# Performance work log

Hardware: AMD Instinct MI355X
Metric: run time of the kernel (lower is better)

## Reference

```python
import jax, jax.numpy as jnp
import numpy as np

N = 50000      # nodes
E = 800000     # edges
MUL = 32       # multiplicity of each irrep (32x0e + 32x1o)
SQRT3 = 3.0 ** 0.5


def setup_inputs() -> dict:
    key = jax.random.key(0)
    k = jax.random.split(key, 7)
    node_features = jax.random.normal(k[0], (N, 4 * MUL), dtype=jnp.float32)  # [N, 32 + 32*3]
    positions = jax.random.normal(k[1], (N, 3), dtype=jnp.float32)
    edge_src = jax.random.randint(k[2], (E,), 0, N, dtype=jnp.int32)
    edge_dst = jax.random.randint(k[3], (E,), 0, N, dtype=jnp.int32)
    tp_weight = jax.random.normal(k[4], (4 * MUL,), dtype=jnp.float32)  # tp.weight_numel = 128
    W_s = jax.random.normal(k[5], (2 * MUL, MUL), dtype=jnp.float32)    # linear: mid 0e (2 blocks) -> out 0e
    W_v = jax.random.normal(k[6], (2 * MUL, MUL), dtype=jnp.float32)    # linear: mid 1o (2 blocks) -> out 1o
    return dict(node_features=node_features, positions=positions,
                edge_src=edge_src, edge_dst=edge_dst,
                tp_weight=tp_weight, W_s=W_s, W_v=W_v)


def reference(node_features, positions, edge_src, edge_dst, tp_weight, W_s, W_v):
    # --- edge vectors and spherical harmonics (normalize=True, 'component') ---
    edge_vec = positions[edge_dst] - positions[edge_src]                       # [E,3]
    unit = edge_vec * jax.lax.rsqrt(jnp.sum(edge_vec * edge_vec, -1, keepdims=True) + 1e-12)
    sh1 = SQRT3 * unit                                                         # l=1 SH, component norm; sh0 == 1
    # --- gather source node features, split irreps ---
    src = node_features[edge_src]                                              # [E,128]
    s = src[:, :MUL]                                                           # [E,32]  scalars 32x0e
    v = src[:, MUL:].reshape(-1, MUL, 3)                                       # [E,32,3] vectors 32x1o
    w0, w1, w2, w3 = jnp.split(tp_weight, 4)                                   # per-path 'uvu' weights (u=32, v=1)
    # --- CG tensor product paths ---
    mid0 = w0 * s                                                              # 0e x 0e -> 0e
    mid1 = (w1 * s)[:, :, None] * sh1[:, None, :]                              # 0e x 1o -> 1o
    mid2 = w2[None, :, None] * v                                               # 1o x 0e -> 1o
    mid3 = w3 * (jnp.einsum('eum,em->eu', v, sh1) / SQRT3)                     # 1o x 1o -> 0e (w3j = delta/sqrt(3))
    messages = jnp.concatenate(
        [mid0, mid1.reshape(-1, 3 * MUL), mid2.reshape(-1, 3 * MUL), mid3], axis=-1)  # [E,256]
    # --- scatter-add messages to destination nodes ---
    agg = jax.ops.segment_sum(messages, edge_dst, num_segments=N)              # [N,256]
    a0 = agg[:, :MUL]
    a1 = agg[:, MUL:4 * MUL].reshape(N, MUL, 3)
    a2 = agg[:, 4 * MUL:7 * MUL].reshape(N, MUL, 3)
    a3 = agg[:, 7 * MUL:]
    # --- equivariant linear mix mid -> out (fan-in normalized per irrep) ---
    inv = np.float32(1.0 / np.sqrt(2 * MUL))
    out_s = (jnp.concatenate([a0, a3], axis=-1) @ W_s) * inv                   # [N,32]
    out_v = jnp.einsum('num,uo->nom', jnp.concatenate([a1, a2], axis=1), W_v) * inv  # [N,32,3]
    return jnp.concatenate([out_s, out_v.reshape(N, 3 * MUL)], axis=-1)        # [N,128]
```

## Files before the change

### kernel.cpp

```cpp
#include <hip/hip_runtime.h>
#include <hip/hip_fp16.h>

#define SQRT3 1.7320508075688772f
#define INV_SQRT3 0.5773502691896258f
#define CAP 64

#define WAVE_SYNC() do { asm volatile("s_waitcnt lgkmcnt(0)" ::: "memory"); \
                         __builtin_amdgcn_wave_barrier(); } while (0)

__global__ void prep_kernel(const float* __restrict__ feat, const float* __restrict__ pos,
                            const float* __restrict__ Ws, const float* __restrict__ Wv,
                            const float* __restrict__ tpw,
                            uint2* __restrict__ featH, float4* __restrict__ pos4,
                            int* __restrict__ cnt,
                            __half2* __restrict__ WS2, __half2* __restrict__ WV2, int N) {
    int i = blockIdx.x * blockDim.x + threadIdx.x;
    int totalF = N * 32;
    if (i < totalF) {
        int node = i >> 5, cl = i & 31;
        const float* fb = feat + (size_t)node * 128;
        float s  = fb[cl];
        float v0 = fb[32 + 3 * cl], v1 = fb[33 + 3 * cl], v2 = fb[34 + 3 * cl];
        __half2 h0 = __floats2half2_rn(s, v0);
        __half2 h1 = __floats2half2_rn(v1, v2);
        uint2 r;
        r.x = *(const unsigned int*)&h0;
        r.y = *(const unsigned int*)&h1;
        featH[i] = r;
        return;
    }
    int j = i - totalF;
    if (j < N) {
        pos4[j] = make_float4(pos[3 * j], pos[3 * j + 1], pos[3 * j + 2], 0.f);
        cnt[j] = 0;
        return;
    }
    int k = j - N;
    if (k < 1024) {
        int u2 = k >> 5, c = k & 31;
        int ua = 2 * u2, ub = 2 * u2 + 1;
        auto fs = [&](int u) {
            float w = Ws[u * 32 + c];
            return (u < 32) ? 0.125f * tpw[u] * w
                            : 0.125f * tpw[96 + (u - 32)] * INV_SQRT3 * w;
        };
        auto fv = [&](int u) {
            float w = Wv[u * 32 + c];
            return (u < 32) ? 0.125f * tpw[32 + u] * w
                            : 0.125f * tpw[64 + (u - 32)] * w;
        };
        WS2[k] = __floats2half2_rn(fs(ua), fs(ub));
        WV2[k] = __floats2half2_rn(fv(ua), fv(ub));
    }
}

__global__ void scatter_kernel(const int* __restrict__ esrc, const int* __restrict__ edst,
                               int* __restrict__ cnt, int* __restrict__ csrP, int E) {
    int t = blockIdx.x * blockDim.x + threadIdx.x;
    int e0 = t * 4;
    if (e0 + 4 <= E) {
        int4 s4 = *(const int4*)(esrc + e0);
        int4 d4 = *(const int4*)(edst + e0);
        int p;
        p = atomicAdd(&cnt[d4.x], 1); if (p < CAP) csrP[(size_t)d4.x * CAP + p] = s4.x;
        p = atomicAdd(&cnt[d4.y], 1); if (p < CAP) csrP[(size_t)d4.y * CAP + p] = s4.y;
        p = atomicAdd(&cnt[d4.z], 1); if (p < CAP) csrP[(size_t)d4.z * CAP + p] = s4.z;
        p = atomicAdd(&cnt[d4.w], 1); if (p < CAP) csrP[(size_t)d4.w * CAP + p] = s4.w;
    } else {
        for (int e = e0; e < E; ++e) {
            int d = edst[e];
            int p = atomicAdd(&cnt[d], 1);
            if (p < CAP) csrP[(size_t)d * CAP + p] = esrc[e];
        }
    }
}


__global__ __launch_bounds__(256) void node_kernel(
    const uint2* __restrict__ featH, const float4* __restrict__ pos4,
    const int* __restrict__ csrP, const int* __restrict__ cnt,
    const __half2* __restrict__ WS2, const __half2* __restrict__ WV2,
    float* __restrict__ out, int N)
{
    __shared__ float4 geom[4][64];
    __shared__ float  sS[4][68], sX[4][68], sY[4][68], sZ[4][68];
    int lane = threadIdx.x & 63;
    int w    = threadIdx.x >> 6;
    int node = blockIdx.x * 4 + w;
    if (node >= N) return;

    int deg = cnt[node];
    int len = deg < CAP ? deg : CAP;
    int half = lane >> 5;
    int cl   = lane & 31;

    float4 pd = pos4[node];

    if (lane < len) {
        int s = csrP[(size_t)node * CAP + lane];
        float4 ps = pos4[s];
        float ex = pd.x - ps.x, ey = pd.y - ps.y, ez = pd.z - ps.z;
        float rr = SQRT3 * rsqrtf(ex * ex + ey * ey + ez * ez + 1e-12f);
        geom[w][lane] = make_float4(rr * ex, rr * ey, rr * ez, __int_as_float(s));
    }
    WAVE_SYNC();

    float A0 = 0.f, A1x = 0.f, A1y = 0.f, A1z = 0.f;
    float V0 = 0.f, V1 = 0.f, V2 = 0.f, T3 = 0.f;

    int even = len & ~1;
    #pragma unroll 4
    for (int m = 0; m < even; m += 2) {
        float4 g = geom[w][m + half];
        int si = __float_as_int(g.w);
        uint2 fr = featH[(size_t)si * 32 + cl];
        float2 lo = __half22float2(*(const __half2*)&fr.x);
        float2 hi = __half22float2(*(const __half2*)&fr.y);
        A0 += lo.x;
        A1x = fmaf(lo.x, g.x, A1x); A1y = fmaf(lo.x, g.y, A1y); A1z = fmaf(lo.x, g.z, A1z);
        V0 += lo.y; V1 += hi.x; V2 += hi.y;
        T3 = fmaf(lo.y, g.x, fmaf(hi.x, g.y, fmaf(hi.y, g.z, T3)));
    }
    if (len & 1) {
        if (half == 0) {
            float4 g = geom[w][len - 1];
            int si = __float_as_int(g.w);
            uint2 fr = featH[(size_t)si * 32 + cl];
            float2 lo = __half22float2(*(const __half2*)&fr.x);
            float2 hi = __half22float2(*(const __half2*)&fr.y);
            A0 += lo.x;
            A1x = fmaf(lo.x, g.x, A1x); A1y = fmaf(lo.x, g.y, A1y); A1z = fmaf(lo.x, g.z, A1z);
            V0 += lo.y; V1 += hi.x; V2 += hi.y;
            T3 = fmaf(lo.y, g.x, fmaf(hi.x, g.y, fmaf(hi.y, g.z, T3)));
        }
    }

    A0 += __shfl_xor(A0, 32);  A1x += __shfl_xor(A1x, 32);
    A1y += __shfl_xor(A1y, 32); A1z += __shfl_xor(A1z, 32);
    V0 += __shfl_xor(V0, 32);  V1 += __shfl_xor(V1, 32);
    V2 += __shfl_xor(V2, 32);  T3 += __shfl_xor(T3, 32);

    int k = half ? (32 + cl) : cl;
    sS[w][k] = half ? T3 : A0;
    sX[w][k] = half ? V0 : A1x;
    sY[w][k] = half ? V1 : A1y;
    sZ[w][k] = half ? V2 : A1z;
    WAVE_SYNC();

    size_t ob = (size_t)node * 128;
    #pragma unroll
    for (int t = 0; t < 2; ++t) {
        int j = lane + 64 * t;
        const float *ap;
        const __half2 *wp2;
        if (j < 32) {
            ap = sS[w]; wp2 = WS2 + j;
        } else {
            int v = j - 32;
            int o = v / 3, mm = v - 3 * o;
            ap = (mm == 0) ? sX[w] : (mm == 1) ? sY[w] : sZ[w];
            wp2 = WV2 + o;
        }
        float r = 0.f;
        #pragma unroll
        for (int q = 0; q < 16; ++q) {
            float4 a = *(const float4*)(ap + 4 * q);
            float2 w0 = __half22float2(wp2[(2 * q)     * 32]);
            float2 w1 = __half22float2(wp2[(2 * q + 1) * 32]);
            r = fmaf(a.x, w0.x, r); r = fmaf(a.y, w0.y, r);
            r = fmaf(a.z, w1.x, r); r = fmaf(a.w, w1.y, r);
        }
        out[ob + j] = r;
    }
}

extern "C" void kernel_launch(void* const* d_in, const int* in_sizes, int n_in,
                              void* d_out, int out_size, void* d_ws, size_t ws_size,
                              hipStream_t stream) {
    const float* feat = (const float*)d_in[0];
    const float* pos  = (const float*)d_in[1];
    const int*   esrc = (const int*)d_in[2];
    const int*   edst = (const int*)d_in[3];
    const float* tpw  = (const float*)d_in[4];
    const float* Ws   = (const float*)d_in[5];
    const float* Wv   = (const float*)d_in[6];
    float* out = (float*)d_out;

    int N = in_sizes[0] / 128;
    int E = in_sizes[2];

    uint2*   featH = (uint2*)d_ws;
    float4*  pos4  = (float4*)(featH + (size_t)N * 32);
    int*     csrP  = (int*)(pos4 + N);
    int*     cnt   = csrP + (size_t)N * CAP;
    __half2* WS2   = (__half2*)(cnt + N);
    __half2* WV2   = WS2 + 1024;

    const int tb = 256;
    int prepTot = N * 32 + N + 1024;
    int ebk = (E / 4 + tb) / tb;
    prep_kernel<<<(prepTot + tb - 1) / tb, tb, 0, stream>>>(feat, pos, Ws, Wv, tpw,
                                                            featH, pos4, cnt, WS2, WV2, N);
    scatter_kernel<<<ebk, tb, 0, stream>>>(esrc, edst, cnt, csrP, E);
    node_kernel<<<(N + 3) / 4, 256, 0, stream>>>(featH, pos4, csrP, cnt, WS2, WV2, out, N);
}
```

Baseline: 107.5 us.

## Process two destination nodes per wave with zero-padded gather loop

Each wave now handles two destination nodes at once. Edge lists are padded to a multiple of 8 using a dummy zero feature row at index N, so the inner loop runs without odd-length tails and issues two independent feature gathers per iteration. This raises memory-level parallelism and removes divergent tail handling. In exchange it does wasted work when the two nodes have unequal degrees, uses more registers and shared memory, and halves the number of blocks.

```diff
diff --git a/kernel.cpp b/kernel.cpp
--- a/kernel.cpp
+++ b/kernel.cpp
@@ -30,6 +30,8 @@
         return;
     }
     int j = i - totalF;
+    if (j < 32) { featH[totalF + j] = make_uint2(0u, 0u); return; }
+    j -= 32;
     if (j < N) {
         pos4[j] = make_float4(pos[3 * j], pos[3 * j + 1], pos[3 * j + 2], 0.f);
         cnt[j] = 0;
@@ -82,95 +84,127 @@
     const __half2* __restrict__ WS2, const __half2* __restrict__ WV2,
     float* __restrict__ out, int N)
 {
-    __shared__ float4 geom[4][64];
-    __shared__ float  sS[4][68], sX[4][68], sY[4][68], sZ[4][68];
+    __shared__ float4 geom[4][2][64];
+    __shared__ float  sS[4][2][68], sX[4][2][68], sY[4][2][68], sZ[4][2][68];
     int lane = threadIdx.x & 63;
     int w    = threadIdx.x >> 6;
-    int node = blockIdx.x * 4 + w;
-    if (node >= N) return;
-
-    int deg = cnt[node];
-    int len = deg < CAP ? deg : CAP;
+    int n0   = blockIdx.x * 8 + 2 * w;
+    if (n0 >= N) return;
+    int n1   = n0 + 1;
+    bool has1 = n1 < N;
+
+    int len0 = cnt[n0]; len0 = len0 < CAP ? len0 : CAP;
+    int len1 = 0;
+    if (has1) { len1 = cnt[n1]; len1 = len1 < CAP ? len1 : CAP; }
+    int lmax = len0 > len1 ? len0 : len1;
+    int lenP = (lmax + 7) & ~7;
     int half = lane >> 5;
     int cl   = lane & 31;
 
-    float4 pd = pos4[node];
-
-    if (lane < len) {
-        int s = csrP[(size_t)node * CAP + lane];
-        float4 ps = pos4[s];
-        float ex = pd.x - ps.x, ey = pd.y - ps.y, ez = pd.z - ps.z;
-        float rr = SQRT3 * rsqrtf(ex * ex + ey * ey + ez * ez + 1e-12f);
-        geom[w][lane] = make_float4(rr * ex, rr * ey, rr * ez, __int_as_float(s));
+    {
+        float4 pd = pos4[n0];
+        if (lane < len0) {
+            int s = csrP[(size_t)n0 * CAP + lane];
+            float4 ps = pos4[s];
+            float ex = pd.x - ps.x, ey = pd.y - ps.y, ez = pd.z - ps.z;
+            float rr = SQRT3 * rsqrtf(ex * ex + ey * ey + ez * ez + 1e-12f);
+            geom[w][0][lane] = make_float4(rr * ex, rr * ey, rr * ez, __int_as_float(s));
+        } else {
+            geom[w][0][lane] = make_float4(0.f, 0.f, 0.f, __int_as_float(N));
+        }
+    }
+    if (has1) {
+        float4 pd = pos4[n1];
+        if (lane < len1) {
+            int s = csrP[(size_t)n1 * CAP + lane];
+            float4 ps = pos4[s];
+            float ex = pd.x - ps.x, ey = pd.y - ps.y, ez = pd.z - ps.z;
+            float rr = SQRT3 * rsqrtf(ex * ex + ey * ey + ez * ez + 1e-12f);
+            geom[w][1][lane] = make_float4(rr * ex, rr * ey, rr * ez, __int_as_float(s));
+        } else {
+            geom[w][1][lane] = make_float4(0.f, 0.f, 0.f, __int_as_float(N));
+        }
+    } else {
+        geom[w][1][lane] = make_float4(0.f, 0.f, 0.f, __int_as_float(N));
     }
     WAVE_SYNC();
 
-    float A0 = 0.f, A1x = 0.f, A1y = 0.f, A1z = 0.f;
-    float V0 = 0.f, V1 = 0.f, V2 = 0.f, T3 = 0.f;
-
-    int even = len & ~1;
+    float A0a = 0.f, A1xa = 0.f, A1ya = 0.f, A1za = 0.f;
+    float V0a = 0.f, V1a = 0.f, V2a = 0.f, T3a = 0.f;
+    float A0b = 0.f, A1xb = 0.f, A1yb = 0.f, A1zb = 0.f;
+    float V0b = 0.f, V1b = 0.f, V2b = 0.f, T3b = 0.f;
+
     #pragma unroll 4
-    for (int m = 0; m < even; m += 2) {
-        float4 g = geom[w][m + half];
-        int si = __float_as_int(g.w);
-        uint2 fr = featH[(size_t)si * 32 + cl];
-        float2 lo = __half22float2(*(const __half2*)&fr.x);
-        float2 hi = __half22float2(*(const __half2*)&fr.y);
-        A0 += lo.x;
-        A1x = fmaf(lo.x, g.x, A1x); A1y = fmaf(lo.x, g.y, A1y); A1z = fmaf(lo.x, g.z, A1z);
-        V0 += lo.y; V1 += hi.x; V2 += hi.y;
-        T3 = fmaf(lo.y, g.x, fmaf(hi.x, g.y, fmaf(hi.y, g.z, T3)));
-    }
-    if (len & 1) {
-        if (half == 0) {
-            float4 g = geom[w][len - 1];
-            int si = __float_as_int(g.w);
-            uint2 fr = featH[(size_t)si * 32 + cl];
-            float2 lo = __half22float2(*(const __half2*)&fr.x);
-            float2 hi = __half22float2(*(const __half2*)&fr.y);
-            A0 += lo.x;
-            A1x = fmaf(lo.x, g.x, A1x); A1y = fmaf(lo.x, g.y, A1y); A1z = fmaf(lo.x, g.z, A1z);
-            V0 += lo.y; V1 += hi.x; V2 += hi.y;
-            T3 = fmaf(lo.y, g.x, fmaf(hi.x, g.y, fmaf(hi.y, g.z, T3)));
-        }
-    }
-
-    A0 += __shfl_xor(A0, 32);  A1x += __shfl_xor(A1x, 32);
-    A1y += __shfl_xor(A1y, 32); A1z += __shfl_xor(A1z, 32);
-    V0 += __shfl_xor(V0, 32);  V1 += __shfl_xor(V1, 32);
-    V2 += __shfl_xor(V2, 32);  T3 += __shfl_xor(T3, 32);
+    for (int m = 0; m + 2 <= lenP; m += 2) {
+        int e = m + half;
+        float4 g0 = geom[w][0][e];
+        float4 g1 = geom[w][1][e];
+        int s0 = __float_as_int(g0.w);
+        int s1 = __float_as_int(g1.w);
+        uint2 f0 = featH[(size_t)s0 * 32 + cl];
+        uint2 f1 = featH[(size_t)s1 * 32 + cl];
+        float2 lo0 = __half22float2(*(const __half2*)&f0.x);
+        float2 hi0 = __half22float2(*(const __half2*)&f0.y);
+        float2 lo1 = __half22float2(*(const __half2*)&f1.x);
+        float2 hi1 = __half22float2(*(const __half2*)&f1.y);
+        A0a += lo0.x;
+        A1xa = fmaf(lo0.x, g0.x, A1xa); A1ya = fmaf(lo0.x, g0.y, A1ya); A1za = fmaf(lo0.x, g0.z, A1za);
+        V0a += lo0.y; V1a += hi0.x; V2a += hi0.y;
+        T3a = fmaf(lo0.y, g0.x, fmaf(hi0.x, g0.y, fmaf(hi0.y, g0.z, T3a)));
+        A0b += lo1.x;
+        A1xb = fmaf(lo1.x, g1.x, A1xb); A1yb = fmaf(lo1.x, g1.y, A1yb); A1zb = fmaf(lo1.x, g1.z, A1zb);
+        V0b += lo1.y; V1b += hi1.x; V2b += hi1.y;
+        T3b = fmaf(lo1.y, g1.x, fmaf(hi1.x, g1.y, fmaf(hi1.y, g1.z, T3b)));
+    }
+
+    A0a += __shfl_xor(A0a, 32);  A1xa += __shfl_xor(A1xa, 32);
+    A1ya += __shfl_xor(A1ya, 32); A1za += __shfl_xor(A1za, 32);
+    V0a += __shfl_xor(V0a, 32);  V1a += __shfl_xor(V1a, 32);
+    V2a += __shfl_xor(V2a, 32);  T3a += __shfl_xor(T3a, 32);
+    A0b += __shfl_xor(A0b, 32);  A1xb += __shfl_xor(A1xb, 32);
+    A1yb += __shfl_xor(A1yb, 32); A1zb += __shfl_xor(A1zb, 32);
+    V0b += __shfl_xor(V0b, 32);  V1b += __shfl_xor(V1b, 32);
+    V2b += __shfl_xor(V2b, 32);  T3b += __shfl_xor(T3b, 32);
 
     int k = half ? (32 + cl) : cl;
-    sS[w][k] = half ? T3 : A0;
-    sX[w][k] = half ? V0 : A1x;
-    sY[w][k] = half ? V1 : A1y;
-    sZ[w][k] = half ? V2 : A1z;
+    sS[w][0][k] = half ? T3a : A0a;
+    sX[w][0][k] = half ? V0a : A1xa;
+    sY[w][0][k] = half ? V1a : A1ya;
+    sZ[w][0][k] = half ? V2a : A1za;
+    sS[w][1][k] = half ? T3b : A0b;
+    sX[w][1][k] = half ? V0b : A1xb;
+    sY[w][1][k] = half ? V1b : A1yb;
+    sZ[w][1][k] = half ? V2b : A1zb;
     WAVE_SYNC();
 
-    size_t ob = (size_t)node * 128;
     #pragma unroll
-    for (int t = 0; t < 2; ++t) {
-        int j = lane + 64 * t;
-        const float *ap;
-        const __half2 *wp2;
-        if (j < 32) {
-            ap = sS[w]; wp2 = WS2 + j;
-        } else {
-            int v = j - 32;
-            int o = v / 3, mm = v - 3 * o;
-            ap = (mm == 0) ? sX[w] : (mm == 1) ? sY[w] : sZ[w];
-            wp2 = WV2 + o;
-        }
-        float r = 0.f;
+    for (int ni = 0; ni < 2; ++ni) {
+        if (ni == 1 && !has1) break;
+        size_t ob = (size_t)(n0 + ni) * 128;
         #pragma unroll
-        for (int q = 0; q < 16; ++q) {
-            float4 a = *(const float4*)(ap + 4 * q);
-            float2 w0 = __half22float2(wp2[(2 * q)     * 32]);
-            float2 w1 = __half22float2(wp2[(2 * q + 1) * 32]);
-            r = fmaf(a.x, w0.x, r); r = fmaf(a.y, w0.y, r);
-            r = fmaf(a.z, w1.x, r); r = fmaf(a.w, w1.y, r);
-        }
-        out[ob + j] = r;
+        for (int t = 0; t < 2; ++t) {
+            int j = lane + 64 * t;
+            const float *ap;
+            const __half2 *wp2;
+            if (j < 32) {
+                ap = sS[w][ni]; wp2 = WS2 + j;
+            } else {
+                int v = j - 32;
+                int o = v / 3, mm = v - 3 * o;
+                ap = (mm == 0) ? sX[w][ni] : (mm == 1) ? sY[w][ni] : sZ[w][ni];
+                wp2 = WV2 + o;
+            }
+            float r = 0.f;
+            #pragma unroll
+            for (int q = 0; q < 16; ++q) {
+                float4 a = *(const float4*)(ap + 4 * q);
+                float2 w0 = __half22float2(wp2[(2 * q)     * 32]);
+                float2 w1 = __half22float2(wp2[(2 * q + 1) * 32]);
+                r = fmaf(a.x, w0.x, r); r = fmaf(a.y, w0.y, r);
+                r = fmaf(a.z, w1.x, r); r = fmaf(a.w, w1.y, r);
+            }
+            out[ob + j] = r;
+        }
     }
 }
 
@@ -190,17 +224,17 @@
     int E = in_sizes[2];
 
     uint2*   featH = (uint2*)d_ws;
-    float4*  pos4  = (float4*)(featH + (size_t)N * 32);
+    float4*  pos4  = (float4*)(featH + (size_t)(N + 1) * 32);
     int*     csrP  = (int*)(pos4 + N);
     int*     cnt   = csrP + (size_t)N * CAP;
     __half2* WS2   = (__half2*)(cnt + N);
     __half2* WV2   = WS2 + 1024;
 
     const int tb = 256;
-    int prepTot = N * 32 + N + 1024;
+    int prepTot = N * 32 + 32 + N + 1024;
     int ebk = (E / 4 + tb) / tb;
     prep_kernel<<<(prepTot + tb - 1) / tb, tb, 0, stream>>>(feat, pos, Ws, Wv, tpw,
                                                             featH, pos4, cnt, WS2, WV2, N);
     scatter_kernel<<<ebk, tb, 0, stream>>>(esrc, edst, cnt, csrP, E);
-    node_kernel<<<(N + 3) / 4, 256, 0, stream>>>(featH, pos4, csrP, cnt, WS2, WV2, out, N);
-}
+    node_kernel<<<(N + 7) / 8, 256, 0, stream>>>(featH, pos4, csrP, cnt, WS2, WV2, out, N);
+}
```

Result: slower. 113.8 us (+5.8%).
